# Optimization experiments

Hardware: AMD Instinct MI355X
Metric: run time of the kernel (lower is better)

The kernel has to match this reference:

```python
import jax, jax.numpy as jnp
import numpy as np

N_NODES = 10000
N_EDGES = 160000
N_GRAPHS = 64
X_IN = 128
HID = 64
EDGE_DIM = 16
HEADS = 4
# (in_dim, out_dim_per_head) for the 3 TransformerConv layers (concat=False)
DIMS = [(X_IN, HID), (HID, 2 * HID), (2 * HID, HID)]
WNAMES = [f"{n}{l}" for l in (1, 2, 3) for n in ("wq", "bq", "wk", "bk", "wv", "bv", "we", "ws", "bs")]


def setup_inputs() -> dict:
    key = jax.random.key(0)
    ks = iter(jax.random.split(key, 64))
    inp = {}
    inp["x"] = jax.random.normal(next(ks), (N_NODES, X_IN), jnp.float32)
    inp["edge_index"] = jax.random.randint(next(ks), (2, N_EDGES), 0, N_NODES)
    inp["edge_attr"] = jax.random.normal(next(ks), (N_EDGES, EDGE_DIM), jnp.float32)
    inp["batch"] = jnp.sort(jax.random.randint(next(ks), (N_NODES,), 0, N_GRAPHS))
    for l, (din, dout) in enumerate(DIMS, 1):
        hd = HEADS * dout
        for nm, shape in [("wq", (din, hd)), ("wk", (din, hd)), ("wv", (din, hd)),
                          ("we", (EDGE_DIM, hd)), ("ws", (din, dout))]:
            inp[f"{nm}{l}"] = jax.random.normal(next(ks), shape, jnp.float32) * 0.05
        inp[f"bq{l}"] = jnp.zeros((hd,), jnp.float32)
        inp[f"bk{l}"] = jnp.zeros((hd,), jnp.float32)
        inp[f"bv{l}"] = jnp.zeros((hd,), jnp.float32)
        inp[f"bs{l}"] = jnp.zeros((dout,), jnp.float32)
    return inp


def _transformer_conv(x, src, dst, edge_attr, wq, bq, wk, bk, wv, bv, we, ws, bs, dout):
    """PyG TransformerConv, concat=False, root_weight=True, with edge features."""
    N = x.shape[0]
    q = (x @ wq + bq).reshape(N, HEADS, dout)
    k = (x @ wk + bk).reshape(N, HEADS, dout)
    v = (x @ wv + bv).reshape(N, HEADS, dout)
    e = (edge_attr @ we).reshape(-1, HEADS, dout)  # [E, H, C]
    k_j = k[src] + e                               # edge-conditioned keys
    alpha = jnp.einsum("ehd,ehd->eh", q[dst], k_j) * (1.0 / float(dout) ** 0.5)  # [E, H]
    # numerically stable segment softmax over incoming edges of each dst node
    a_max = jax.ops.segment_max(alpha, dst, num_segments=N)
    ex = jnp.exp(alpha - a_max[dst])
    den = jax.ops.segment_sum(ex, dst, num_segments=N)
    attn = ex / den[dst]
    agg = jax.ops.segment_sum((v[src] + e) * attn[..., None], dst, num_segments=N)  # [N, H, C]
    return agg.mean(axis=1) + x @ ws + bs  # concat=False -> head mean; + skip


def _forward(x, edge_attr, edge_index, batch, params):
    src, dst = edge_index[0], edge_index[1]
    h = x
    for l, (_, dout) in enumerate(DIMS, 1):
        p = [params[f"{n}{l}"] for n in ("wq", "bq", "wk", "bk", "wv", "bv", "we", "ws", "bs")]
        h = jax.nn.elu(_transformer_conv(h, src, dst, edge_attr, *p, dout))
    # global mean pool over graphs
    s = jax.ops.segment_sum(h, batch, num_segments=N_GRAPHS)
    cnt = jax.ops.segment_sum(jnp.ones((h.shape[0], 1), h.dtype), batch, num_segments=N_GRAPHS)
    return s / jnp.maximum(cnt, 1.0)


def reference(x, edge_index, edge_attr, batch,
              wq1, bq1, wk1, bk1, wv1, bv1, we1, ws1, bs1,
              wq2, bq2, wk2, bk2, wv2, bv2, we2, ws2, bs2,
              wq3, bq3, wk3, bk3, wv3, bv3, we3, ws3, bs3):
    params = dict(locals())
    return _forward(x, edge_attr, edge_index, batch, params)
```

## Files before the change

### kernel.cpp

```cpp
#include <hip/hip_runtime.h>
#include <hip/hip_fp16.h>
#include <math.h>

#define N_NODES 10000
#define N_EDGES 160000
#define N_GRAPHS 64

using half8 = __attribute__((ext_vector_type(8))) _Float16;
using floatx4 = __attribute__((ext_vector_type(4))) float;

template <int NV> struct KW;
template <> struct KW<1> { using T = uint2; };
template <> struct KW<2> { using T = uint4; };

__device__ inline void cvt_kv(const uint2& w, float4* dst) {
  float2 a = __half22float2(*reinterpret_cast<const __half2*>(&w.x));
  float2 b = __half22float2(*reinterpret_cast<const __half2*>(&w.y));
  dst[0] = make_float4(a.x, a.y, b.x, b.y);
}
__device__ inline void cvt_kv(const uint4& w, float4* dst) {
  float2 a = __half22float2(*reinterpret_cast<const __half2*>(&w.x));
  float2 b = __half22float2(*reinterpret_cast<const __half2*>(&w.y));
  float2 c = __half22float2(*reinterpret_cast<const __half2*>(&w.z));
  float2 d = __half22float2(*reinterpret_cast<const __half2*>(&w.w));
  dst[0] = make_float4(a.x, a.y, b.x, b.y);
  dst[1] = make_float4(c.x, c.y, d.x, d.y);
}

template <int K, int HD, int DOUT>
__global__ __launch_bounds__(256) void gemm_mfma(
    const __half* __restrict__ A, const __half* __restrict__ Wp,
    const float* __restrict__ bias, __half* __restrict__ QS,
    __half* __restrict__ KV, int M) {
  constexpr int QSS = HD + 64 + DOUT;
  constexpr int KVS = 2 * HD;
  constexpr int KS = K / 32;
  __shared__ __half st[64][72];
  const int tid = threadIdx.x;
  const int wave = tid >> 6, lane = tid & 63;
  const int quad = lane >> 4, n16 = lane & 15;
  const int row0 = blockIdx.y * 64;
  const int col0 = blockIdx.x * 64;
  const int nblk0 = blockIdx.x * 4;

  const int arow = min(row0 + wave * 16 + n16, M - 1);
  half8 afrag[KS];
#pragma unroll
  for (int s = 0; s < KS; ++s)
    afrag[s] = *reinterpret_cast<const half8*>(A + (size_t)arow * K + s * 32 + quad * 8);

  floatx4 acc[4];
#pragma unroll
  for (int t = 0; t < 4; ++t) {
    acc[t] = (floatx4){0.f, 0.f, 0.f, 0.f};
#pragma unroll
    for (int s = 0; s < KS; ++s) {
      half8 bf = *reinterpret_cast<const half8*>(
          Wp + (((size_t)(nblk0 + t) * KS + s) * 64 + lane) * 8);
      acc[t] = __builtin_amdgcn_mfma_f32_16x16x32_f16(afrag[s], bf, acc[t], 0, 0, 0);
    }
  }

#pragma unroll
  for (int t = 0; t < 4; ++t) {
    float bv = bias[col0 + t * 16 + n16];
#pragma unroll
    for (int r = 0; r < 4; ++r)
      st[wave * 16 + quad * 4 + r][t * 16 + n16] = __float2half(acc[t][r] + bv);
  }
  __syncthreads();

  __half* dp;
  int colb, stride;
  if (col0 < HD + 64) {
    dp = QS; colb = col0; stride = QSS;
  } else if (col0 < 3 * HD + 64) {
    dp = KV; colb = col0 - HD - 64; stride = KVS;
  } else {
    dp = QS; colb = HD + 64 + (col0 - 3 * HD - 64); stride = QSS;
  }
  for (int c = tid; c < 512; c += 256) {
    int r = c >> 3, seg = c & 7;
    int row = row0 + r;
    if (row < M)
      *reinterpret_cast<uint4*>(dp + (size_t)row * stride + colb + seg * 8) =
          *reinterpret_cast<const uint4*>(&st[r][seg * 8]);
  }
}

__device__ inline void pack_layer(int i, int K, int HD, int DOUT, float scale,
                                  const float* wq, const float* wk,
                                  const float* wv, const float* wsk,
                                  const float* we, const float* bq,
                                  const float* bk, const float* bv,
                                  const float* bs, __half* Wp, float* bcat) {
  const int W = 3 * HD + DOUT + 64;
  const int KS = K / 32;
  if (i < K * W) {
    int j = i & 7, lane = (i >> 3) & 63, fs = i >> 9;
    int nblk = fs / KS, s = fs - nblk * KS;
    int quad = lane >> 4, n = lane & 15;
    int k = s * 32 + quad * 8 + j, c = nblk * 16 + n;
    float v;
    if (c < HD) {
      v = wq[k * HD + c] * scale;
    } else if (c < HD + 64) {
      int gi = c - HD, hh = gi >> 4, d = gi & 15;
      float a = 0.f;
      for (int cc = 0; cc < DOUT; ++cc)
        a += wq[k * HD + hh * DOUT + cc] * we[d * HD + hh * DOUT + cc];
      v = a * scale;
    } else if (c < 2 * HD + 64) {
      v = wk[k * HD + (c - HD - 64)];
    } else if (c < 3 * HD + 64) {
      v = wv[k * HD + (c - 2 * HD - 64)];
    } else {
      v = wsk[k * DOUT + (c - 3 * HD - 64)];
    }
    Wp[i] = __float2half(v);
  } else {
    int c = i - K * W;
    float v;
    if (c < HD) {
      v = bq[c] * scale;
    } else if (c < HD + 64) {
      int gi = c - HD, hh = gi >> 4, d = gi & 15;
      float a = 0.f;
      for (int cc = 0; cc < DOUT; ++cc)
        a += bq[hh * DOUT + cc] * we[d * HD + hh * DOUT + cc];
      v = a * scale;
    } else if (c < 2 * HD + 64) {
      v = bk[c - HD - 64];
    } else if (c < 3 * HD + 64) {
      v = bv[c - 2 * HD - 64];
    } else {
      v = bs[c - 3 * HD - 64];
    }
    bcat[c] = v;
  }
}

#define T1 115584
#define T2 227904
#define T3 343488
#define TCONV (N_NODES * 32)
#define TTOT (T3 + TCONV)

__global__ void pack_all(
    const float* wq1, const float* wk1, const float* wv1, const float* ws1,
    const float* we1, const float* bq1, const float* bk1, const float* bv1,
    const float* bs1,
    const float* wq2, const float* wk2, const float* wv2, const float* ws2,
    const float* we2, const float* bq2, const float* bk2, const float* bv2,
    const float* bs2,
    const float* wq3, const float* wk3, const float* wv3, const float* ws3,
    const float* we3, const float* bq3, const float* bk3, const float* bv3,
    const float* bs3,
    __half* W1, float* b1, __half* W2, float* b2, __half* W3, float* b3,
    const float* x, __half* x16) {
  const float SC1 = 0.125f, SC2 = 0.08838834764831845f;
  for (int i = blockIdx.x * blockDim.x + threadIdx.x; i < TTOT;
       i += gridDim.x * blockDim.x) {
    if (i < T1)
      pack_layer(i, 128, 256, 64, SC1, wq1, wk1, wv1, ws1, we1, bq1, bk1, bv1, bs1, W1, b1);
    else if (i < T2)
      pack_layer(i - T1, 64, 512, 128, SC2, wq2, wk2, wv2, ws2, we2, bq2, bk2, bv2, bs2, W2, b2);
    else if (i < T3)
      pack_layer(i - T2, 128, 256, 64, SC1, wq3, wk3, wv3, ws3, we3, bq3, bk3, bv3, bs3, W3, b3);
    else {
      int k = i - T3;
      float4 v = reinterpret_cast<const float4*>(x)[k];
      __half2* o = reinterpret_cast<__half2*>(x16) + 2 * k;
      o[0] = __floats2half2_rn(v.x, v.y);
      o[1] = __floats2half2_rn(v.z, v.w);
    }
  }
}

__global__ void count_dst(const int* __restrict__ dst, int* __restrict__ cnt) {
  int e = blockIdx.x * blockDim.x + threadIdx.x;
  if (e < N_EDGES) atomicAdd(&cnt[dst[e]], 1);
}

__global__ __launch_bounds__(1024) void scan_offs(const int* __restrict__ cnt,
                                                  int* __restrict__ offs,
                                                  int* __restrict__ perm) {
  __shared__ int part[1024];
  __shared__ int hist[256], hstart[256], hcur[256];
  const int t = threadIdx.x;
  const int chunk = (N_NODES + 1023) / 1024;
  const int b = t * chunk;
  const int e = min(N_NODES, b + chunk);
  if (t < 256) { hist[t] = 0; hcur[t] = 0; }
  __syncthreads();
  int s = 0;
  for (int i = b; i < e; ++i) {
    int d = cnt[i];
    s += d;
    atomicAdd(&hist[min(d, 255)], 1);
  }
  part[t] = s;
  __syncthreads();
  for (int off = 1; off < 1024; off <<= 1) {
    int v = (t >= off) ? part[t - off] : 0;
    __syncthreads();
    part[t] += v;
    __syncthreads();
  }
  if (t == 0) {
    int acc = 0;
    for (int bk = 255; bk >= 0; --bk) { hstart[bk] = acc; acc += hist[bk]; }
    offs[N_NODES] = part[1023];
  }
  __syncthreads();
  int pre = (t == 0) ? 0 : part[t - 1];
  for (int i = b; i < e; ++i) {
    offs[i] = pre;
    int d = cnt[i];
    pre += d;
    int bkt = min(d, 255);
    int pos = hstart[bkt] + atomicAdd(&hcur[bkt], 1);
    perm[pos] = i;
  }
}

__global__ void scatter_csr(const int* __restrict__ src, const int* __restrict__ dst,
                            const float* __restrict__ edge_attr,
                            const int* __restrict__ offs, int* __restrict__ cursor,
                            int* __restrict__ csr_src, float* __restrict__ csr_ea) {
  int e = blockIdx.x * blockDim.x + threadIdx.x;
  if (e < N_EDGES) {
    int d = dst[e];
    int pos = offs[d] + atomicAdd(&cursor[d], 1);
    csr_src[pos] = src[e];
    float4* o4 = reinterpret_cast<float4*>(csr_ea + (size_t)pos * 16);
    const float4* s4 = reinterpret_cast<const float4*>(edge_attr + (size_t)e * 16);
    o4[0] = s4[0]; o4[1] = s4[1]; o4[2] = s4[2]; o4[3] = s4[3];
  }
}

template <int DOUT, bool W32>
__global__ __launch_bounds__(128) void edge_attn(
    const __half* __restrict__ QS, const __half* __restrict__ KV,
    const float* __restrict__ we, const int* __restrict__ csr_src,
    const float* __restrict__ csr_ea, const int* __restrict__ offs,
    const int* __restrict__ perm, float* __restrict__ out,
    __half* __restrict__ out16) {
  constexpr int HD = 4 * DOUT;
  constexpr int QSS = HD + 64 + DOUT;
  constexpr int KVS = 2 * HD;
  constexpr int NV = DOUT / 64;
  using KWT = typename KW<NV>::T;

  const int lane = threadIdx.x & 63;
  const int h = lane >> 4, t16 = lane & 15;
  const int n = perm[blockIdx.x * 2 + (threadIdx.x >> 6)];
  const int c0 = t16 * 4 * NV;

  const __half* base = QS + (size_t)n * QSS;
  float4 q[NV], acc[NV];
  {
    KWT qw = *reinterpret_cast<const KWT*>(base + h * DOUT + c0);
    cvt_kv(qw, q);
  }
#pragma unroll
  for (int v = 0; v < NV; ++v) acc[v] = make_float4(0.f, 0.f, 0.f, 0.f);
  const float g = __half2float(base[HD + h * 16 + t16]);

  float lsum = 0.f, tacc = 0.f;

  const int s0 = offs[n], s1 = offs[n + 1];

  int sjA[4], sjB[4];
  float eaA[4], eaB[4];
  KWT krA[4], vrA[4], krB[4], vrB[4];

  auto load_grp = [&](int bi, int (&sj)[4], float (&ea)[4], KWT (&kr)[4],
                      KWT (&vr)[4]) {
#pragma unroll
    for (int j = 0; j < 4; ++j) sj[j] = csr_src[bi + j];
#pragma unroll
    for (int j = 0; j < 4; ++j) ea[j] = csr_ea[(size_t)(bi + j) * 16 + t16];
#pragma unroll
    for (int j = 0; j < 4; ++j) {
      const __half* rb = KV + (size_t)sj[j] * KVS + h * DOUT + c0;
      kr[j] = *reinterpret_cast<const KWT*>(rb);
      vr[j] = *reinterpret_cast<const KWT*>(rb + HD);
    }
  };

  auto compute_grp = [&](float (&ea)[4], KWT (&kr)[4], KWT (&vr)[4]) {
    float a[4];
#pragma unroll
    for (int j = 0; j < 4; ++j) {
      float4 kk[NV];
      cvt_kv(kr[j], kk);
      float p = ea[j] * g;
#pragma unroll
      for (int v = 0; v < NV; ++v)
        p += q[v].x * kk[v].x + q[v].y * kk[v].y + q[v].z * kk[v].z +
             q[v].w * kk[v].w;
      a[j] = p;
    }
#pragma unroll
    for (int j = 0; j < 4; ++j) {
      a[j] += __shfl_xor(a[j], 1);
      a[j] += __shfl_xor(a[j], 2);
      a[j] += __shfl_xor(a[j], 4);
      a[j] += __shfl_xor(a[j], 8);
    }
    float p0 = __expf(a[0]), p1 = __expf(a[1]);
    float p2 = __expf(a[2]), p3 = __expf(a[3]);
    lsum += p0 + p1 + p2 + p3;
    tacc += p0 * ea[0] + p1 * ea[1] + p2 * ea[2] + p3 * ea[3];
    float pj[4] = {p0, p1, p2, p3};
#pragma unroll
    for (int j = 0; j < 4; ++j) {
      float4 vv[NV];
      cvt_kv(vr[j], vv);
#pragma unroll
      for (int v = 0; v < NV; ++v) {
        acc[v].x += pj[j] * vv[v].x;
        acc[v].y += pj[j] * vv[v].y;
        acc[v].z += pj[j] * vv[v].z;
        acc[v].w += pj[j] * vv[v].w;
      }
    }
  };

  int ii = s0;
  const int end_full = s0 + ((s1 - s0) & ~3);
  if (ii < end_full) {
    load_grp(ii, sjA, eaA, krA, vrA);
    for (;;) {
      int nx = ii + 4;
      if (nx >= end_full) { compute_grp(eaA, krA, vrA); ii = nx; break; }
      load_grp(nx, sjB, eaB, krB, vrB);
      compute_grp(eaA, krA, vrA);
      ii = nx; nx = ii + 4;
      if (nx >= end_full) { compute_grp(eaB, krB, vrB); ii = nx; break; }
      load_grp(nx, sjA, eaA, krA, vrA);
      compute_grp(eaB, krB, vrB);
      ii = nx;
    }
  }

  for (; ii < s1; ++ii) {
    int s = csr_src[ii];
    float ea0 = csr_ea[(size_t)ii * 16 + t16];
    const __half* rb = KV + (size_t)s * KVS + h * DOUT + c0;
    KWT kw = *reinterpret_cast<const KWT*>(rb);
    KWT vw = *reinterpret_cast<const KWT*>(rb + HD);
    float4 kk[NV], vv[NV];
    cvt_kv(kw, kk);
    cvt_kv(vw, vv);
    float a = ea0 * g;
#pragma unroll
    for (int v = 0; v < NV; ++v)
      a += q[v].x * kk[v].x + q[v].y * kk[v].y + q[v].z * kk[v].z + q[v].w * kk[v].w;
    a += __shfl_xor(a, 1);
    a += __shfl_xor(a, 2);
    a += __shfl_xor(a, 4);
    a += __shfl_xor(a, 8);
    float p = __expf(a);
    lsum += p;
    tacc += p * ea0;
#pragma unroll
    for (int v = 0; v < NV; ++v) {
      acc[v].x += p * vv[v].x;
      acc[v].y += p * vv[v].y;
      acc[v].z += p * vv[v].z;
      acc[v].w += p * vv[v].w;
    }
  }

  float invl = (lsum > 0.f) ? 1.f / lsum : 0.f;
  float tn = tacc * invl;
  float4 val[NV];
#pragma unroll
  for (int v = 0; v < NV; ++v) {
    val[v].x = acc[v].x * invl; val[v].y = acc[v].y * invl;
    val[v].z = acc[v].z * invl; val[v].w = acc[v].w * invl;
  }
#pragma unroll
  for (int d = 0; d < 16; ++d) {
    float td = __shfl(tn, (lane & 48) | d);
    const float* wb = we + d * HD + h * DOUT + c0;
#pragma unroll
    for (int v = 0; v < NV; ++v) {
      float4 w4 = *reinterpret_cast<const float4*>(wb + 4 * v);
      val[v].x += td * w4.x; val[v].y += td * w4.y;
      val[v].z += td * w4.z; val[v].w += td * w4.w;
    }
  }
#pragma unroll
  for (int v = 0; v < NV; ++v) {
    val[v].x += __shfl_xor(val[v].x, 16); val[v].x += __shfl_xor(val[v].x, 32);
    val[v].y += __shfl_xor(val[v].y, 16); val[v].y += __shfl_xor(val[v].y, 32);
    val[v].z += __shfl_xor(val[v].z, 16); val[v].z += __shfl_xor(val[v].z, 32);
    val[v].w += __shfl_xor(val[v].w, 16); val[v].w += __shfl_xor(val[v].w, 32);
  }
  if (h == 0) {
    KWT sw = *reinterpret_cast<const KWT*>(base + HD + 64 + c0);
    float4 sk[NV];
    cvt_kv(sw, sk);
#pragma unroll
    for (int v = 0; v < NV; ++v) {
      float4 o;
      o.x = 0.25f * val[v].x + sk[v].x;
      o.y = 0.25f * val[v].y + sk[v].y;
      o.z = 0.25f * val[v].z + sk[v].z;
      o.w = 0.25f * val[v].w + sk[v].w;
      o.x = (o.x > 0.f) ? o.x : expm1f(o.x);
      o.y = (o.y > 0.f) ? o.y : expm1f(o.y);
      o.z = (o.z > 0.f) ? o.z : expm1f(o.z);
      o.w = (o.w > 0.f) ? o.w : expm1f(o.w);
      if (W32)
        *reinterpret_cast<float4*>(out + (size_t)n * DOUT + c0 + 4 * v) = o;
      __half2* o16 = reinterpret_cast<__half2*>(out16 + (size_t)n * DOUT + c0 + 4 * v);
      o16[0] = __floats2half2_rn(o.x, o.y);
      o16[1] = __floats2half2_rn(o.z, o.w);
    }
  }
}

__device__ inline int lower_bound(const int* b, int n, int v) {
  int lo = 0, hi = n;
  while (lo < hi) {
    int mid = (lo + hi) >> 1;
    if (b[mid] < v) lo = mid + 1; else hi = mid;
  }
  return lo;
}

__global__ __launch_bounds__(256) void pool_all(const float* __restrict__ h,
                                                const int* __restrict__ batch,
                                                float* __restrict__ out) {
  const int g = blockIdx.x;
  const int start = lower_bound(batch, N_NODES, g);
  const int end = lower_bound(batch, N_NODES, g + 1);
  const int c = threadIdx.x & 63, j = threadIdx.x >> 6;
  float s = 0.f;
  for (int n = start + j; n < end; n += 4) s += h[(size_t)n * 64 + c];
  __shared__ float red[4][64];
  red[j][c] = s;
  __syncthreads();
  if (j == 0) {
    float tot = red[0][c] + red[1][c] + red[2][c] + red[3][c];
    out[g * 64 + c] = tot / (float)max(end - start, 1);
  }
}

extern "C" void kernel_launch(void* const* d_in, const int* in_sizes, int n_in,
                              void* d_out, int out_size, void* d_ws, size_t ws_size,
                              hipStream_t stream) {
  const float* x = (const float*)d_in[0];
  const int* edge_index = (const int*)d_in[1];
  const float* edge_attr = (const float*)d_in[2];
  const int* batch = (const int*)d_in[3];
  const int* srcp = edge_index;
  const int* dstp = edge_index + N_EDGES;

  const bool dict_order = in_sizes[5] > 1024;
  const float *wq[3], *wk[3], *wv[3], *wep[3], *wsk[3], *bq[3], *bk[3], *bv[3], *bs[3];
  for (int L = 0; L < 3; ++L) {
    int b = 4 + L * 9;
    if (dict_order) {
      wq[L] = (const float*)d_in[b + 0];
      wk[L] = (const float*)d_in[b + 1];
      wv[L] = (const float*)d_in[b + 2];
      wep[L] = (const float*)d_in[b + 3];
      wsk[L] = (const float*)d_in[b + 4];
      bq[L] = (const float*)d_in[b + 5];
      bk[L] = (const float*)d_in[b + 6];
      bv[L] = (const float*)d_in[b + 7];
      bs[L] = (const float*)d_in[b + 8];
    } else {
      wq[L] = (const float*)d_in[b + 0];
      bq[L] = (const float*)d_in[b + 1];
      wk[L] = (const float*)d_in[b + 2];
      bk[L] = (const float*)d_in[b + 3];
      wv[L] = (const float*)d_in[b + 4];
      bv[L] = (const float*)d_in[b + 5];
      wep[L] = (const float*)d_in[b + 6];
      wsk[L] = (const float*)d_in[b + 7];
      bs[L] = (const float*)d_in[b + 8];
    }
  }

  char* p = (char*)d_ws;
  __half* qs = (__half*)p;    p += (size_t)N_NODES * 704 * 2;
  __half* kv = (__half*)p;    p += (size_t)N_NODES * 1024 * 2;
  float* h1 = (float*)p;      p += (size_t)N_NODES * 64 * 4;
  __half* x16 = (__half*)p;   p += (size_t)N_NODES * 128 * 2;
  __half* h16 = (__half*)p;   p += (size_t)N_NODES * 128 * 2;
  __half* W1 = (__half*)p;    p += 128 * 896 * 2;
  __half* W2 = (__half*)p;    p += 64 * 1728 * 2;
  __half* W3 = (__half*)p;    p += 128 * 896 * 2;
  float* b1 = (float*)p;      p += 896 * 4;
  float* b2 = (float*)p;      p += 1728 * 4;
  float* b3 = (float*)p;      p += 896 * 4;
  float* csr_ea = (float*)p;  p += (size_t)N_EDGES * 16 * 4;
  int* cnt = (int*)p;         p += N_NODES * 4;
  int* cursor = (int*)p;      p += N_NODES * 4;
  int* offs = (int*)p;        p += (N_NODES + 1) * 4;
  int* perm = (int*)p;        p += N_NODES * 4;
  int* csr_src = (int*)p;     p += N_EDGES * 4;

  pack_all<<<1024, 256, 0, stream>>>(
      wq[0], wk[0], wv[0], wsk[0], wep[0], bq[0], bk[0], bv[0], bs[0],
      wq[1], wk[1], wv[1], wsk[1], wep[1], bq[1], bk[1], bv[1], bs[1],
      wq[2], wk[2], wv[2], wsk[2], wep[2], bq[2], bk[2], bv[2], bs[2],
      W1, b1, W2, b2, W3, b3, x, x16);

  hipMemsetAsync(cnt, 0, 2 * N_NODES * sizeof(int), stream);
  count_dst<<<(N_EDGES + 255) / 256, 256, 0, stream>>>(dstp, cnt);
  scan_offs<<<1, 1024, 0, stream>>>(cnt, offs, perm);
  scatter_csr<<<(N_EDGES + 255) / 256, 256, 0, stream>>>(srcp, dstp, edge_attr,
                                                         offs, cursor, csr_src, csr_ea);

  const int MT = (N_NODES + 63) / 64;
  gemm_mfma<128, 256, 64><<<dim3(896 / 64, MT), 256, 0, stream>>>(x16, W1, b1, qs,
                                                                  kv, N_NODES);
  edge_attn<64, false><<<N_NODES / 2, 128, 0, stream>>>(qs, kv, wep[0], csr_src,
                                                        csr_ea, offs, perm, h1, h16);
  gemm_mfma<64, 512, 128><<<dim3(1728 / 64, MT), 256, 0, stream>>>(h16, W2, b2, qs,
                                                                   kv, N_NODES);
  edge_attn<128, false><<<N_NODES / 2, 128, 0, stream>>>(qs, kv, wep[1], csr_src,
                                                         csr_ea, offs, perm, h1, h16);
  gemm_mfma<128, 256, 64><<<dim3(896 / 64, MT), 256, 0, stream>>>(h16, W3, b3, qs,
                                                                  kv, N_NODES);
  edge_attn<64, true><<<N_NODES / 2, 128, 0, stream>>>(qs, kv, wep[2], csr_src,
                                                       csr_ea, offs, perm, h1, x16);

  pool_all<<<N_GRAPHS, 256, 0, stream>>>(h1, batch, (float*)d_out);
}
```

Before: 334.7 us.

## Fuse weight packing and CSR build into one cooperative kernel; drop degree sort

```diff
diff --git a/kernel.cpp b/kernel.cpp
--- a/kernel.cpp
+++ b/kernel.cpp
@@ -1,6 +1,9 @@
 #include <hip/hip_runtime.h>
+#include <hip/hip_cooperative_groups.h>
 #include <hip/hip_fp16.h>
 #include <math.h>
+
+namespace cg = cooperative_groups;
 
 #define N_NODES 10000
 #define N_EDGES 160000
@@ -146,95 +149,83 @@
 #define TCONV (N_NODES * 32)
 #define TTOT (T3 + TCONV)
 
-__global__ void pack_all(
-    const float* wq1, const float* wk1, const float* wv1, const float* ws1,
-    const float* we1, const float* bq1, const float* bk1, const float* bv1,
-    const float* bs1,
-    const float* wq2, const float* wk2, const float* wv2, const float* ws2,
-    const float* we2, const float* bq2, const float* bk2, const float* bv2,
-    const float* bs2,
-    const float* wq3, const float* wk3, const float* wv3, const float* ws3,
-    const float* we3, const float* bq3, const float* bk3, const float* bv3,
-    const float* bs3,
-    __half* W1, float* b1, __half* W2, float* b2, __half* W3, float* b3,
-    const float* x, __half* x16) {
+struct PrepArgs {
+  const float *wq1, *wk1, *wv1, *ws1, *we1, *bq1, *bk1, *bv1, *bs1;
+  const float *wq2, *wk2, *wv2, *ws2, *we2, *bq2, *bk2, *bv2, *bs2;
+  const float *wq3, *wk3, *wv3, *ws3, *we3, *bq3, *bk3, *bv3, *bs3;
+  __half *W1; float *b1; __half *W2; float *b2; __half *W3; float *b3;
+  const float* x; __half* x16;
+  const int *src, *dst;
+  const float* edge_attr;
+  int *cnt, *cursor, *offs, *csr_src;
+  float* csr_ea;
+  int *bsum, *bbase;
+};
+
+__global__ __launch_bounds__(256) void prep_all(PrepArgs a) {
+  cg::grid_group grid = cg::this_grid();
+  const int tid = blockIdx.x * 256 + threadIdx.x;
+  const int NT = gridDim.x * 256;
   const float SC1 = 0.125f, SC2 = 0.08838834764831845f;
-  for (int i = blockIdx.x * blockDim.x + threadIdx.x; i < TTOT;
-       i += gridDim.x * blockDim.x) {
+
+  for (int i = tid; i < 2 * N_NODES; i += NT) a.cnt[i] = 0;
+  for (int i = tid; i < TTOT; i += NT) {
     if (i < T1)
-      pack_layer(i, 128, 256, 64, SC1, wq1, wk1, wv1, ws1, we1, bq1, bk1, bv1, bs1, W1, b1);
+      pack_layer(i, 128, 256, 64, SC1, a.wq1, a.wk1, a.wv1, a.ws1, a.we1,
+                 a.bq1, a.bk1, a.bv1, a.bs1, a.W1, a.b1);
     else if (i < T2)
-      pack_layer(i - T1, 64, 512, 128, SC2, wq2, wk2, wv2, ws2, we2, bq2, bk2, bv2, bs2, W2, b2);
+      pack_layer(i - T1, 64, 512, 128, SC2, a.wq2, a.wk2, a.wv2, a.ws2, a.we2,
+                 a.bq2, a.bk2, a.bv2, a.bs2, a.W2, a.b2);
     else if (i < T3)
-      pack_layer(i - T2, 128, 256, 64, SC1, wq3, wk3, wv3, ws3, we3, bq3, bk3, bv3, bs3, W3, b3);
+      pack_layer(i - T2, 128, 256, 64, SC1, a.wq3, a.wk3, a.wv3, a.ws3, a.we3,
+                 a.bq3, a.bk3, a.bv3, a.bs3, a.W3, a.b3);
     else {
       int k = i - T3;
-      float4 v = reinterpret_cast<const float4*>(x)[k];
-      __half2* o = reinterpret_cast<__half2*>(x16) + 2 * k;
+      float4 v = reinterpret_cast<const float4*>(a.x)[k];
+      __half2* o = reinterpret_cast<__half2*>(a.x16) + 2 * k;
       o[0] = __floats2half2_rn(v.x, v.y);
       o[1] = __floats2half2_rn(v.z, v.w);
     }
   }
-}
-
-__global__ void count_dst(const int* __restrict__ dst, int* __restrict__ cnt) {
-  int e = blockIdx.x * blockDim.x + threadIdx.x;
-  if (e < N_EDGES) atomicAdd(&cnt[dst[e]], 1);
-}
-
-__global__ __launch_bounds__(1024) void scan_offs(const int* __restrict__ cnt,
-                                                  int* __restrict__ offs,
-                                                  int* __restrict__ perm) {
-  __shared__ int part[1024];
-  __shared__ int hist[256], hstart[256], hcur[256];
-  const int t = threadIdx.x;
-  const int chunk = (N_NODES + 1023) / 1024;
-  const int b = t * chunk;
-  const int e = min(N_NODES, b + chunk);
-  if (t < 256) { hist[t] = 0; hcur[t] = 0; }
-  __syncthreads();
-  int s = 0;
-  for (int i = b; i < e; ++i) {
-    int d = cnt[i];
-    s += d;
-    atomicAdd(&hist[min(d, 255)], 1);
-  }
-  part[t] = s;
-  __syncthreads();
-  for (int off = 1; off < 1024; off <<= 1) {
-    int v = (t >= off) ? part[t - off] : 0;
+  grid.sync();
+
+  for (int e = tid; e < N_EDGES; e += NT) atomicAdd(&a.cnt[a.dst[e]], 1);
+  grid.sync();
+
+  const int i0 = blockIdx.x * 40;
+  const int i1 = min(N_NODES, i0 + 40);
+  if (threadIdx.x == 0) {
+    int s = 0;
+    for (int i = i0; i < i1; ++i) { a.offs[i] = s; s += a.cnt[i]; }
+    a.bsum[blockIdx.x] = s;
+  }
+  grid.sync();
+
+  if (blockIdx.x == 0) {
+    __shared__ int sc[256];
+    int t = threadIdx.x;
+    sc[t] = a.bsum[t];
     __syncthreads();
-    part[t] += v;
-    __syncthreads();
-  }
-  if (t == 0) {
-    int acc = 0;
-    for (int bk = 255; bk >= 0; --bk) { hstart[bk] = acc; acc += hist[bk]; }
-    offs[N_NODES] = part[1023];
-  }
-  __syncthreads();
-  int pre = (t == 0) ? 0 : part[t - 1];
-  for (int i = b; i < e; ++i) {
-    offs[i] = pre;
-    int d = cnt[i];
-    pre += d;
-    int bkt = min(d, 255);
-    int pos = hstart[bkt] + atomicAdd(&hcur[bkt], 1);
-    perm[pos] = i;
-  }
-}
-
-__global__ void scatter_csr(const int* __restrict__ src, const int* __restrict__ dst,
-                            const float* __restrict__ edge_attr,
-                            const int* __restrict__ offs, int* __restrict__ cursor,
-                            int* __restrict__ csr_src, float* __restrict__ csr_ea) {
-  int e = blockIdx.x * blockDim.x + threadIdx.x;
-  if (e < N_EDGES) {
-    int d = dst[e];
-    int pos = offs[d] + atomicAdd(&cursor[d], 1);
-    csr_src[pos] = src[e];
-    float4* o4 = reinterpret_cast<float4*>(csr_ea + (size_t)pos * 16);
-    const float4* s4 = reinterpret_cast<const float4*>(edge_attr + (size_t)e * 16);
+    for (int off = 1; off < 256; off <<= 1) {
+      int v = (t >= off) ? sc[t - off] : 0;
+      __syncthreads();
+      sc[t] += v;
+      __syncthreads();
+    }
+    a.bbase[t] = (t == 0) ? 0 : sc[t - 1];
+    if (t == 255) a.offs[N_NODES] = sc[255];
+  }
+  grid.sync();
+
+  if (threadIdx.x < (i1 - i0)) a.offs[i0 + threadIdx.x] += a.bbase[blockIdx.x];
+  grid.sync();
+
+  for (int e = tid; e < N_EDGES; e += NT) {
+    int d = a.dst[e];
+    int pos = a.offs[d] + atomicAdd(&a.cursor[d], 1);
+    a.csr_src[pos] = a.src[e];
+    float4* o4 = reinterpret_cast<float4*>(a.csr_ea + (size_t)pos * 16);
+    const float4* s4 = reinterpret_cast<const float4*>(a.edge_attr + (size_t)e * 16);
     o4[0] = s4[0]; o4[1] = s4[1]; o4[2] = s4[2]; o4[3] = s4[3];
   }
 }
@@ -244,8 +235,7 @@
     const __half* __restrict__ QS, const __half* __restrict__ KV,
     const float* __restrict__ we, const int* __restrict__ csr_src,
     const float* __restrict__ csr_ea, const int* __restrict__ offs,
-    const int* __restrict__ perm, float* __restrict__ out,
-    __half* __restrict__ out16) {
+    float* __restrict__ out, __half* __restrict__ out16) {
   constexpr int HD = 4 * DOUT;
   constexpr int QSS = HD + 64 + DOUT;
   constexpr int KVS = 2 * HD;
@@ -254,7 +244,7 @@
 
   const int lane = threadIdx.x & 63;
   const int h = lane >> 4, t16 = lane & 15;
-  const int n = perm[blockIdx.x * 2 + (threadIdx.x >> 6)];
+  const int n = blockIdx.x * 2 + (threadIdx.x >> 6);
   const int c0 = t16 * 4 * NV;
 
   const __half* base = QS + (size_t)n * QSS;
@@ -504,34 +494,39 @@
   int* cnt = (int*)p;         p += N_NODES * 4;
   int* cursor = (int*)p;      p += N_NODES * 4;
   int* offs = (int*)p;        p += (N_NODES + 1) * 4;
-  int* perm = (int*)p;        p += N_NODES * 4;
   int* csr_src = (int*)p;     p += N_EDGES * 4;
-
-  pack_all<<<1024, 256, 0, stream>>>(
-      wq[0], wk[0], wv[0], wsk[0], wep[0], bq[0], bk[0], bv[0], bs[0],
-      wq[1], wk[1], wv[1], wsk[1], wep[1], bq[1], bk[1], bv[1], bs[1],
-      wq[2], wk[2], wv[2], wsk[2], wep[2], bq[2], bk[2], bv[2], bs[2],
-      W1, b1, W2, b2, W3, b3, x, x16);
-
-  hipMemsetAsync(cnt, 0, 2 * N_NODES * sizeof(int), stream);
-  count_dst<<<(N_EDGES + 255) / 256, 256, 0, stream>>>(dstp, cnt);
-  scan_offs<<<1, 1024, 0, stream>>>(cnt, offs, perm);
-  scatter_csr<<<(N_EDGES + 255) / 256, 256, 0, stream>>>(srcp, dstp, edge_attr,
-                                                         offs, cursor, csr_src, csr_ea);
+  int* bsum = (int*)p;        p += 256 * 4;
+  int* bbase = (int*)p;       p += 256 * 4;
+
+  PrepArgs pa;
+  pa.wq1 = wq[0]; pa.wk1 = wk[0]; pa.wv1 = wv[0]; pa.ws1 = wsk[0]; pa.we1 = wep[0];
+  pa.bq1 = bq[0]; pa.bk1 = bk[0]; pa.bv1 = bv[0]; pa.bs1 = bs[0];
+  pa.wq2 = wq[1]; pa.wk2 = wk[1]; pa.wv2 = wv[1]; pa.ws2 = wsk[1]; pa.we2 = wep[1];
+  pa.bq2 = bq[1]; pa.bk2 = bk[1]; pa.bv2 = bv[1]; pa.bs2 = bs[1];
+  pa.wq3 = wq[2]; pa.wk3 = wk[2]; pa.wv3 = wv[2]; pa.ws3 = wsk[2]; pa.we3 = wep[2];
+  pa.bq3 = bq[2]; pa.bk3 = bk[2]; pa.bv3 = bv[2]; pa.bs3 = bs[2];
+  pa.W1 = W1; pa.b1 = b1; pa.W2 = W2; pa.b2 = b2; pa.W3 = W3; pa.b3 = b3;
+  pa.x = x; pa.x16 = x16;
+  pa.src = srcp; pa.dst = dstp; pa.edge_attr = edge_attr;
+  pa.cnt = cnt; pa.cursor = cursor; pa.offs = offs; pa.csr_src = csr_src;
+  pa.csr_ea = csr_ea; pa.bsum = bsum; pa.bbase = bbase;
+  void* prep_args[] = {&pa};
+  hipLaunchCooperativeKernel(reinterpret_cast<const void*>(prep_all), dim3(256),
+                             dim3(256), prep_args, 0, stream);
 
   const int MT = (N_NODES + 63) / 64;
   gemm_mfma<128, 256, 64><<<dim3(896 / 64, MT), 256, 0, stream>>>(x16, W1, b1, qs,
                                                                   kv, N_NODES);
   edge_attn<64, false><<<N_NODES / 2, 128, 0, stream>>>(qs, kv, wep[0], csr_src,
-                                                        csr_ea, offs, perm, h1, h16);
+                                                        csr_ea, offs, h1, h16);
   gemm_mfma<64, 512, 128><<<dim3(1728 / 64, MT), 256, 0, stream>>>(h16, W2, b2, qs,
                                                                    kv, N_NODES);
   edge_attn<128, false><<<N_NODES / 2, 128, 0, stream>>>(qs, kv, wep[1], csr_src,
-                                                         csr_ea, offs, perm, h1, h16);
+                                                         csr_ea, offs, h1, h16);
   gemm_mfma<128, 256, 64><<<dim3(896 / 64, MT), 256, 0, stream>>>(h16, W3, b3, qs,
                                                                   kv, N_NODES);
   edge_attn<64, true><<<N_NODES / 2, 128, 0, stream>>>(qs, kv, wep[2], csr_src,
-                                                       csr_ea, offs, perm, h1, x16);
+                                                       csr_ea, offs, h1, x16);
 
   pool_all<<<N_GRAPHS, 256, 0, stream>>>(h1, batch, (float*)d_out);
 }
```

After: 517.7 us. +54.7%, slower.

## Build deterministic sorted CSR, fuse dst counting into pack, prefetch GEMM B fragments

Applied to the files above, without the earlier changes.

```diff
diff --git a/kernel.cpp b/kernel.cpp
--- a/kernel.cpp
+++ b/kernel.cpp
@@ -49,16 +49,22 @@
   for (int s = 0; s < KS; ++s)
     afrag[s] = *reinterpret_cast<const half8*>(A + (size_t)arow * K + s * 32 + quad * 8);
 
+  half8 bfr[4][KS];
+#pragma unroll
+  for (int t = 0; t < 4; ++t)
+#pragma unroll
+    for (int s = 0; s < KS; ++s)
+      bfr[t][s] = *reinterpret_cast<const half8*>(
+          Wp + (((size_t)(nblk0 + t) * KS + s) * 64 + lane) * 8);
+
   floatx4 acc[4];
 #pragma unroll
   for (int t = 0; t < 4; ++t) {
     acc[t] = (floatx4){0.f, 0.f, 0.f, 0.f};
 #pragma unroll
-    for (int s = 0; s < KS; ++s) {
-      half8 bf = *reinterpret_cast<const half8*>(
-          Wp + (((size_t)(nblk0 + t) * KS + s) * 64 + lane) * 8);
-      acc[t] = __builtin_amdgcn_mfma_f32_16x16x32_f16(afrag[s], bf, acc[t], 0, 0, 0);
-    }
+    for (int s = 0; s < KS; ++s)
+      acc[t] = __builtin_amdgcn_mfma_f32_16x16x32_f16(afrag[s], bfr[t][s], acc[t],
+                                                      0, 0, 0);
   }
 
 #pragma unroll
@@ -157,7 +163,7 @@
     const float* we3, const float* bq3, const float* bk3, const float* bv3,
     const float* bs3,
     __half* W1, float* b1, __half* W2, float* b2, __half* W3, float* b3,
-    const float* x, __half* x16) {
+    const float* x, __half* x16, const int* dst, int* cnt) {
   const float SC1 = 0.125f, SC2 = 0.08838834764831845f;
   for (int i = blockIdx.x * blockDim.x + threadIdx.x; i < TTOT;
        i += gridDim.x * blockDim.x) {
@@ -175,11 +181,9 @@
       o[1] = __floats2half2_rn(v.z, v.w);
     }
   }
-}
-
-__global__ void count_dst(const int* __restrict__ dst, int* __restrict__ cnt) {
-  int e = blockIdx.x * blockDim.x + threadIdx.x;
-  if (e < N_EDGES) atomicAdd(&cnt[dst[e]], 1);
+  for (int e = blockIdx.x * blockDim.x + threadIdx.x; e < N_EDGES;
+       e += gridDim.x * blockDim.x)
+    atomicAdd(&cnt[dst[e]], 1);
 }
 
 __global__ __launch_bounds__(1024) void scan_offs(const int* __restrict__ cnt,
@@ -224,19 +228,38 @@
   }
 }
 
-__global__ void scatter_csr(const int* __restrict__ src, const int* __restrict__ dst,
-                            const float* __restrict__ edge_attr,
-                            const int* __restrict__ offs, int* __restrict__ cursor,
-                            int* __restrict__ csr_src, float* __restrict__ csr_ea) {
+__global__ void scatter_eidx(const int* __restrict__ dst,
+                             const int* __restrict__ offs, int* __restrict__ cursor,
+                             int* __restrict__ eidx) {
   int e = blockIdx.x * blockDim.x + threadIdx.x;
   if (e < N_EDGES) {
     int d = dst[e];
-    int pos = offs[d] + atomicAdd(&cursor[d], 1);
-    csr_src[pos] = src[e];
-    float4* o4 = reinterpret_cast<float4*>(csr_ea + (size_t)pos * 16);
-    const float4* s4 = reinterpret_cast<const float4*>(edge_attr + (size_t)e * 16);
-    o4[0] = s4[0]; o4[1] = s4[1]; o4[2] = s4[2]; o4[3] = s4[3];
-  }
+    eidx[offs[d] + atomicAdd(&cursor[d], 1)] = e;
+  }
+}
+
+__global__ void sort_fix(const int* __restrict__ offs, int* __restrict__ eidx) {
+  int n = blockIdx.x * blockDim.x + threadIdx.x;
+  if (n >= N_NODES) return;
+  int s0 = offs[n], s1 = offs[n + 1];
+  for (int i = s0 + 1; i < s1; ++i) {
+    int v = eidx[i];
+    int j = i - 1;
+    while (j >= s0 && eidx[j] > v) { eidx[j + 1] = eidx[j]; --j; }
+    eidx[j + 1] = v;
+  }
+}
+
+__global__ void gather_csr(const int* __restrict__ eidx, const int* __restrict__ src,
+                           const float* __restrict__ edge_attr,
+                           int* __restrict__ csr_src, float* __restrict__ csr_ea) {
+  int i = blockIdx.x * blockDim.x + threadIdx.x;
+  if (i >= N_EDGES * 4) return;
+  int pos = i >> 2, seg = i & 3;
+  int e = eidx[pos];
+  reinterpret_cast<float4*>(csr_ea)[pos * 4 + seg] =
+      reinterpret_cast<const float4*>(edge_attr)[e * 4 + seg];
+  if (seg == 0) csr_src[pos] = src[e];
 }
 
 template <int DOUT, bool W32>
@@ -506,18 +529,19 @@
   int* offs = (int*)p;        p += (N_NODES + 1) * 4;
   int* perm = (int*)p;        p += N_NODES * 4;
   int* csr_src = (int*)p;     p += N_EDGES * 4;
-
+  int* eidx = (int*)p;        p += N_EDGES * 4;
+
+  hipMemsetAsync(cnt, 0, 2 * N_NODES * sizeof(int), stream);
   pack_all<<<1024, 256, 0, stream>>>(
       wq[0], wk[0], wv[0], wsk[0], wep[0], bq[0], bk[0], bv[0], bs[0],
       wq[1], wk[1], wv[1], wsk[1], wep[1], bq[1], bk[1], bv[1], bs[1],
       wq[2], wk[2], wv[2], wsk[2], wep[2], bq[2], bk[2], bv[2], bs[2],
-      W1, b1, W2, b2, W3, b3, x, x16);
-
-  hipMemsetAsync(cnt, 0, 2 * N_NODES * sizeof(int), stream);
-  count_dst<<<(N_EDGES + 255) / 256, 256, 0, stream>>>(dstp, cnt);
+      W1, b1, W2, b2, W3, b3, x, x16, dstp, cnt);
   scan_offs<<<1, 1024, 0, stream>>>(cnt, offs, perm);
-  scatter_csr<<<(N_EDGES + 255) / 256, 256, 0, stream>>>(srcp, dstp, edge_attr,
-                                                         offs, cursor, csr_src, csr_ea);
+  scatter_eidx<<<(N_EDGES + 255) / 256, 256, 0, stream>>>(dstp, offs, cursor, eidx);
+  sort_fix<<<(N_NODES + 255) / 256, 256, 0, stream>>>(offs, eidx);
+  gather_csr<<<(N_EDGES * 4 + 255) / 256, 256, 0, stream>>>(eidx, srcp, edge_attr,
+                                                            csr_src, csr_ea);
 
   const int MT = (N_NODES + 63) / 64;
   gemm_mfma<128, 256, 64><<<dim3(896 / 64, MT), 256, 0, stream>>>(x16, W1, b1, qs,
```

Measured after the change: 396.5 us. 18.5% more time.
